# Kernel optimization log

Measured on AMD Instinct MI355X. Metric: run time of the kernel, lower is better.

The kernel has to match this reference:

```python
import jax, jax.numpy as jnp
import numpy as np

IN_CH = 64
OUT_CH = 64
SEQ_LEN = 2048
MODES = 64  # modes2 = min(modes1, seq_len//2) = 64
SCALE = 1.0 / (IN_CH * OUT_CH)


def setup_inputs() -> dict:
    key = jax.random.key(0)
    k1, k2, k3 = jax.random.split(key, 3)
    x = jax.random.normal(k1, (32, 8, IN_CH, SEQ_LEN), dtype=jnp.float32)
    # torch.rand(...) complex init scaled by 1/(in*out): real & imag in [0, scale)
    wr = SCALE * jax.random.uniform(k2, (IN_CH, OUT_CH, MODES), dtype=jnp.float32)
    wi = SCALE * jax.random.uniform(k3, (IN_CH, OUT_CH, MODES), dtype=jnp.float32)
    return {"x": x, "wr": wr, "wi": wi}


def reference(x, wr, wi):
    # x: [B, H, E, N] real; weights complex [in, out, modes]
    N = x.shape[-1]
    w = jax.lax.complex(wr, wi)
    x_ft = jnp.fft.rfft(x)                       # [B, H, E, N//2+1] complex64
    a = x_ft[..., :MODES]                        # keep only low modes
    out_low = jnp.einsum('bjix,iox->bjox', a, w)  # per-mode complex matmul
    # zero-fill remaining frequency bins (equivalent to out_ft zeros + slice set)
    pad = N // 2 + 1 - MODES
    out_ft = jnp.pad(out_low, ((0, 0), (0, 0), (0, 0), (0, pad)))
    return jnp.fft.irfft(out_ft, n=N)            # [B, H, out_ch, N] real
```

## Files before the change

### kernel.cpp

```cpp
#include <hip/hip_runtime.h>
#include <hip/hip_bf16.h>


typedef __bf16 bf16x8 __attribute__((ext_vector_type(8)));
typedef float  f32x4  __attribute__((ext_vector_type(4)));

#define SEQ 2048
#define NM2 128
#define KS  2

__device__ __forceinline__ unsigned int rnbf(float f) {
  unsigned int u = __builtin_bit_cast(unsigned int, f);
  return (u + 0x7fffu + ((u >> 16) & 1u)) >> 16;
}
__device__ __forceinline__ unsigned int pack2(float a, float b) {
  return rnbf(a) | (rnbf(b) << 16);
}
__device__ __forceinline__ float frombf(unsigned int lo16_in_place) {
  return __builtin_bit_cast(float, lo16_in_place);
}

typedef const __attribute__((address_space(1))) unsigned int gu32;
typedef __attribute__((address_space(3))) unsigned int lu32;

__global__ __launch_bounds__(256) void k_tables(unsigned short* __restrict__ t1sw,
                                                unsigned short* __restrict__ t2t) {
  int idx = blockIdx.x * 256 + threadIdx.x;
  int k = idx >> 11;
  int n = idx & 2047;
  float rev = (float)((k * n) & 2047) * (1.0f / 2048.0f);
  float s, co;
  asm("v_sin_f32 %0, %1" : "=v"(s)  : "v"(rev));
  asm("v_cos_f32 %0, %1" : "=v"(co) : "v"(rev));
  float ck = (k == 0 ? 1.0f : 2.0f) * (1.0f / 2048.0f);
  int kt = n >> 6, part = (n >> 3) & 7, e = n & 7;
  unsigned base = (unsigned)kt * 16384u + 2u * (unsigned)e;
  unsigned offc = base + (((unsigned)(k * 128 + part * 16)) ^ (((unsigned)k & 7u) << 4));
  int c2 = k + 64;
  unsigned offs = base + (((unsigned)(c2 * 128 + part * 16)) ^ (((unsigned)c2 & 7u) << 4));
  *(unsigned short*)((char*)t1sw + offc) = (unsigned short)rnbf(co);
  *(unsigned short*)((char*)t1sw + offs) = (unsigned short)rnbf(-s);
  t2t[n * NM2 + k]      = (unsigned short)rnbf(ck * co);
  t2t[n * NM2 + k + 64] = (unsigned short)rnbf(-ck * s);
}

__global__ __launch_bounds__(256) void k_gemm1(const float* __restrict__ x,
                                               const unsigned short* __restrict__ t1sw,
                                               unsigned short* __restrict__ P) {
  __shared__ int4 lds4[65536 / 16];
  char* lds = (char*)lds4;
  const int tid = threadIdx.x, wave = tid >> 6, lane = tid & 63;
  const int mtile = blockIdx.x >> 1, ks = blockIdx.x & (KS - 1);
  const int r0 = mtile * 64;
  const int kbase = ks * (SEQ / KS);
  const char* t1base = (const char*)t1sw + (size_t)(kbase >> 6) * 16384;

  const float* xsrc[4];
#pragma unroll
  for (int p = 0; p < 4; ++p) {
    const int row = p * 16 + wave * 4 + (lane >> 4);
    const int u = (lane & 15) ^ (row & 7);
    xsrc[p] = x + (size_t)(r0 + row) * SEQ + kbase + u * 4;
  }

  f32x4 acc[8] = {};

#pragma unroll
  for (int p = 0; p < 4; ++p)
    __builtin_amdgcn_global_load_lds((gu32*)(xsrc[p]),
                                     (lu32*)(lds + p * 4096 + wave * 1024), 16, 0, 0);
#pragma unroll
  for (int p = 0; p < 4; ++p)
    __builtin_amdgcn_global_load_lds((gu32*)(t1base + (p * 256 + tid) * 16),
                                     (lu32*)(lds + 32768 + (p * 256 + wave * 64) * 16), 16, 0, 0);
  asm volatile("s_waitcnt vmcnt(0)" ::: "memory");
  __builtin_amdgcn_s_barrier();

  const int a = wave * 16 + (lane & 15);
  const unsigned xra = (unsigned)(a & 7) << 4;
  const int kg = lane >> 4;

  for (int it = 0; it < 16; ++it) {
    const int cur = it & 1, nxt = cur ^ 1;
    const int xoff = cur * 16384;
    const int toff = 32768 + cur * 16384;
    if (it < 15) {
      const char* tg = t1base + (size_t)(it + 1) * 16384;
#pragma unroll
      for (int p = 0; p < 4; ++p)
        __builtin_amdgcn_global_load_lds((gu32*)(xsrc[p] + (it + 1) * 64),
                                         (lu32*)(lds + nxt * 16384 + p * 4096 + wave * 1024),
                                         16, 0, 0);
#pragma unroll
      for (int p = 0; p < 4; ++p)
        __builtin_amdgcn_global_load_lds((gu32*)(tg + (p * 256 + tid) * 16),
                                         (lu32*)(lds + 32768 + nxt * 16384 + (p * 256 + wave * 64) * 16),
                                         16, 0, 0);
    }
#pragma unroll
    for (int kss = 0; kss < 2; ++kss) {
      const unsigned byte0 = (unsigned)(a * 256 + kss * 128 + kg * 32);
      const f32x4 lo = *(const f32x4*)(lds + xoff + (byte0 ^ xra));
      const f32x4 hi = *(const f32x4*)(lds + xoff + ((byte0 + 16) ^ xra));
      unsigned c0, c1, c2, c3;
      asm("v_cvt_pk_bf16_f32 %0, %1, %2" : "=v"(c0) : "v"(lo[0]), "v"(lo[1]));
      asm("v_cvt_pk_bf16_f32 %0, %1, %2" : "=v"(c1) : "v"(lo[2]), "v"(lo[3]));
      asm("v_cvt_pk_bf16_f32 %0, %1, %2" : "=v"(c2) : "v"(hi[0]), "v"(hi[1]));
      asm("v_cvt_pk_bf16_f32 %0, %1, %2" : "=v"(c3) : "v"(hi[2]), "v"(hi[3]));
      uint4 pk; pk.x = c0; pk.y = c1; pk.z = c2; pk.w = c3;
      const bf16x8 av = __builtin_bit_cast(bf16x8, pk);
#pragma unroll
      for (int t = 0; t < 8; ++t) {
        const int col = t * 16 + (lane & 15);
        const bf16x8 bv = *(const bf16x8*)(lds + toff +
            ((col * 128 + kss * 64 + kg * 16) ^ ((unsigned)(col & 7) << 4)));
        acc[t] = __builtin_amdgcn_mfma_f32_16x16x32_bf16(bv, av, acc[t], 0, 0, 0);
      }
    }
    asm volatile("s_waitcnt vmcnt(0)" ::: "memory");
    __builtin_amdgcn_s_barrier();
  }
  unsigned short* Pout = P + (size_t)ks * (16384 * NM2);
  const int row = r0 + wave * 16 + (lane & 15);
#pragma unroll
  for (int t = 0; t < 8; ++t) {
    const int col0 = t * 16 + kg * 4;
    uint2 v; v.x = pack2(acc[t][0], acc[t][1]); v.y = pack2(acc[t][2], acc[t][3]);
    *(uint2*)(Pout + (size_t)row * NM2 + col0) = v;
  }
}

__global__ __launch_bounds__(256) void k_stage2(const unsigned short* __restrict__ P,
                                                const float* __restrict__ wr,
                                                const float* __restrict__ wi,
                                                unsigned short* __restrict__ Bx) {
  __shared__ float sA[4][64][64];
  const int b = blockIdx.x;
  const int bjc = b >> 2, oh = (b >> 1) & 1, kh = b & 1;
  const int k0 = kh * 32;
  const int tid = threadIdx.x;
#pragma unroll
  for (int p = 0; p < 16; ++p) {
    int fidx = tid + 256 * p;
    int row_lin = fidx >> 4, q = fidx & 15;
    int col = (q < 8) ? (k0 + q * 4) : (64 + k0 + (q - 8) * 4);
    const unsigned short* base = P + (size_t)(bjc * 256 + row_lin) * NM2 + col;
    f32x4 v = {};
#pragma unroll
    for (int s = 0; s < KS; ++s) {
      uint2 u = *(const uint2*)(base + (size_t)s * (16384 * NM2));
      v[0] += frombf(u.x << 16);
      v[1] += frombf(u.x & 0xffff0000u);
      v[2] += frombf(u.y << 16);
      v[3] += frombf(u.y & 0xffff0000u);
    }
    *(f32x4*)(&sA[row_lin >> 6][row_lin & 63][q * 4]) = v;
  }
  __syncthreads();
  const int o_l = tid >> 3, kg = tid & 7;
  const int o = oh * 32 + o_l;
  const int kb = k0 + kg * 4;
  f32x4 accr[4] = {};
  f32x4 acci[4] = {};
  for (int i = 0; i < 64; ++i) {
    f32x4 wrv = *(const f32x4*)(wr + (i * 64 + o) * 64 + kb);
    f32x4 wiv = *(const f32x4*)(wi + (i * 64 + o) * 64 + kb);
#pragma unroll
    for (int bj = 0; bj < 4; ++bj) {
      f32x4 ar = *(const f32x4*)(&sA[bj][i][kg * 4]);
      f32x4 ai = *(const f32x4*)(&sA[bj][i][32 + kg * 4]);
#pragma unroll
      for (int kk = 0; kk < 4; ++kk) {
        accr[bj][kk] += ar[kk] * wrv[kk] - ai[kk] * wiv[kk];
        acci[bj][kk] += ar[kk] * wiv[kk] + ai[kk] * wrv[kk];
      }
    }
  }
#pragma unroll
  for (int bj = 0; bj < 4; ++bj) {
    const int r = (bjc * 4 + bj) * 64 + o;
    uint2 vr; vr.x = pack2(accr[bj][0], accr[bj][1]); vr.y = pack2(accr[bj][2], accr[bj][3]);
    uint2 vi; vi.x = pack2(acci[bj][0], acci[bj][1]); vi.y = pack2(acci[bj][2], acci[bj][3]);
    *(uint2*)(Bx + (size_t)r * NM2 + kb)      = vr;
    *(uint2*)(Bx + (size_t)r * NM2 + 64 + kb) = vi;
  }
}

__global__ __launch_bounds__(256) void k_gemm2(const unsigned short* __restrict__ Bx,
                                               const unsigned short* __restrict__ t2t,
                                               float* __restrict__ out) {
  __shared__ int4 lds4[65536 / 16];
  char* lds = (char*)lds4;
  const int tid = threadIdx.x, wave = tid >> 6, lane = tid & 63;
  const int swz = (blockIdx.x & 7) * 256 + (blockIdx.x >> 3);
  const int mb = swz >> 4, nb = swz & 15;
  const int r0 = mb * 128, n0 = nb * 128;
#pragma unroll
  for (int p = 0; p < 8; ++p) {
    int seg = tid + 256 * p;
    int row = seg >> 4, part = seg & 15;
    unsigned sw = (unsigned)((row * 256 + part * 16) ^ ((row & 7) << 4));
    int4 va = *(const int4*)(Bx + (size_t)(r0 + row) * NM2 + part * 8);
    *(int4*)(lds + sw) = va;
    int4 vb = *(const int4*)(t2t + (size_t)(n0 + row) * NM2 + part * 8);
    *(int4*)(lds + 32768 + sw) = vb;
  }
  __syncthreads();
  f32x4 acc[2][8] = {};
#pragma unroll
  for (int ks = 0; ks < 4; ++ks) {
    const int ar0 = wave * 32 + (lane & 15);
    const int ar1 = ar0 + 16;
    const int koff = ks * 64 + (lane >> 4) * 16;
    bf16x8 a0 = *(const bf16x8*)(lds + ((ar0 * 256 + koff) ^ ((unsigned)(ar0 & 7) << 4)));
    bf16x8 a1 = *(const bf16x8*)(lds + ((ar1 * 256 + koff) ^ ((unsigned)(ar1 & 7) << 4)));
#pragma unroll
    for (int t = 0; t < 8; ++t) {
      const int col = t * 16 + (lane & 15);
      bf16x8 bv = *(const bf16x8*)(lds + 32768 + ((col * 256 + koff) ^ ((unsigned)(col & 7) << 4)));
      acc[0][t] = __builtin_amdgcn_mfma_f32_16x16x32_bf16(a0, bv, acc[0][t], 0, 0, 0);
      acc[1][t] = __builtin_amdgcn_mfma_f32_16x16x32_bf16(a1, bv, acc[1][t], 0, 0, 0);
    }
  }
#pragma unroll
  for (int m = 0; m < 2; ++m) {
#pragma unroll
    for (int j = 0; j < 4; ++j) {
      const int row = r0 + wave * 32 + m * 16 + (lane >> 4) * 4 + j;
#pragma unroll
      for (int t = 0; t < 8; ++t) {
        const int col = n0 + t * 16 + (lane & 15);
        out[(size_t)row * SEQ + col] = acc[m][t][j];
      }
    }
  }
}

extern "C" void kernel_launch(void* const* d_in, const int* in_sizes, int n_in,
                              void* d_out, int out_size, void* d_ws, size_t ws_size,
                              hipStream_t stream) {
  const float* x  = (const float*)d_in[0];
  const float* wr = (const float*)d_in[1];
  const float* wi = (const float*)d_in[2];
  float* out = (float*)d_out;
  char* ws = (char*)d_ws;
  unsigned short* t1sw = (unsigned short*)(ws);
  unsigned short* t2t  = (unsigned short*)(ws + 524288);
  unsigned short* P    = (unsigned short*)(ws + 1048576);
  unsigned short* Bx   = (unsigned short*)(ws + 1048576 + (size_t)KS * 16384 * NM2 * 2);

  k_tables<<<dim3(512),      dim3(256), 0, stream>>>(t1sw, t2t);
  k_gemm1 <<<dim3(256 * KS), dim3(256), 0, stream>>>(x, t1sw, P);
  k_stage2<<<dim3(256),      dim3(256), 0, stream>>>(P, wr, wi, Bx);
  k_gemm2 <<<dim3(2048),     dim3(256), 0, stream>>>(Bx, t2t, out);
}
```

Before: 89.48 us.

## Pre-swizzle gemm2 operands in global memory and load them directly to LDS

The Bx and t2 tables are now written in a tile-contiguous, pre-swizzled layout that matches the LDS image k_gemm2 needs, with real and imaginary halves in separate 16KB blocks. k_gemm2 then fills LDS with global_load_lds DMA instead of register round-trips. It waits only for the first half (vmcnt(8)) before starting MFMAs on it, overlapping the second half's load with compute. This couples the producer layouts tightly to gemm2's tiling and relies on the DMA lane-to-LDS mapping matching the swizzle.

```diff
diff --git a/kernel.cpp b/kernel.cpp
--- a/kernel.cpp
+++ b/kernel.cpp
@@ -24,7 +24,7 @@
 typedef __attribute__((address_space(3))) unsigned int lu32;
 
 __global__ __launch_bounds__(256) void k_tables(unsigned short* __restrict__ t1sw,
-                                                unsigned short* __restrict__ t2t) {
+                                                unsigned short* __restrict__ t2sw) {
   int idx = blockIdx.x * 256 + threadIdx.x;
   int k = idx >> 11;
   int n = idx & 2047;
@@ -33,15 +33,22 @@
   asm("v_sin_f32 %0, %1" : "=v"(s)  : "v"(rev));
   asm("v_cos_f32 %0, %1" : "=v"(co) : "v"(rev));
   float ck = (k == 0 ? 1.0f : 2.0f) * (1.0f / 2048.0f);
-  int kt = n >> 6, part = (n >> 3) & 7, e = n & 7;
-  unsigned base = (unsigned)kt * 16384u + 2u * (unsigned)e;
-  unsigned offc = base + (((unsigned)(k * 128 + part * 16)) ^ (((unsigned)k & 7u) << 4));
-  int c2 = k + 64;
-  unsigned offs = base + (((unsigned)(c2 * 128 + part * 16)) ^ (((unsigned)c2 & 7u) << 4));
-  *(unsigned short*)((char*)t1sw + offc) = (unsigned short)rnbf(co);
-  *(unsigned short*)((char*)t1sw + offs) = (unsigned short)rnbf(-s);
-  t2t[n * NM2 + k]      = (unsigned short)rnbf(ck * co);
-  t2t[n * NM2 + k + 64] = (unsigned short)rnbf(-ck * s);
+  {
+    int kt = n >> 6, part = (n >> 3) & 7, e = n & 7;
+    unsigned base = (unsigned)kt * 16384u + 2u * (unsigned)e;
+    unsigned offc = base + (((unsigned)(k * 128 + part * 16)) ^ (((unsigned)k & 7u) << 4));
+    int c2 = k + 64;
+    unsigned offs = base + (((unsigned)(c2 * 128 + part * 16)) ^ (((unsigned)c2 & 7u) << 4));
+    *(unsigned short*)((char*)t1sw + offc) = (unsigned short)rnbf(co);
+    *(unsigned short*)((char*)t1sw + offs) = (unsigned short)rnbf(-s);
+  }
+  {
+    int tile = n >> 7, rl = n & 127;
+    unsigned rowbase = (unsigned)tile * 32768u + (unsigned)rl * 128u;
+    unsigned kpart = ((((unsigned)(k >> 3)) * 16u) ^ (((unsigned)rl & 7u) << 4)) + 2u * ((unsigned)k & 7u);
+    *(unsigned short*)((char*)t2sw + rowbase + kpart)          = (unsigned short)rnbf(ck * co);
+    *(unsigned short*)((char*)t2sw + rowbase + 16384u + kpart) = (unsigned short)rnbf(-ck * s);
+  }
 }
 
 __global__ __launch_bounds__(256) void k_gemm1(const float* __restrict__ x,
@@ -133,7 +140,7 @@
 __global__ __launch_bounds__(256) void k_stage2(const unsigned short* __restrict__ P,
                                                 const float* __restrict__ wr,
                                                 const float* __restrict__ wi,
-                                                unsigned short* __restrict__ Bx) {
+                                                char* __restrict__ Bxsw) {
   __shared__ float sA[4][64][64];
   const int b = blockIdx.x;
   const int bjc = b >> 2, oh = (b >> 1) & 1, kh = b & 1;
@@ -179,15 +186,18 @@
 #pragma unroll
   for (int bj = 0; bj < 4; ++bj) {
     const int r = (bjc * 4 + bj) * 64 + o;
+    const int tile = r >> 7, rl = r & 127;
+    char* bb = Bxsw + (size_t)tile * 32768 + (size_t)rl * 128;
+    const unsigned kp = ((((unsigned)kb >> 3) * 16u) ^ (((unsigned)rl & 7u) << 4)) + 2u * ((unsigned)kb & 7u);
     uint2 vr; vr.x = pack2(accr[bj][0], accr[bj][1]); vr.y = pack2(accr[bj][2], accr[bj][3]);
     uint2 vi; vi.x = pack2(acci[bj][0], acci[bj][1]); vi.y = pack2(acci[bj][2], acci[bj][3]);
-    *(uint2*)(Bx + (size_t)r * NM2 + kb)      = vr;
-    *(uint2*)(Bx + (size_t)r * NM2 + 64 + kb) = vi;
-  }
-}
-
-__global__ __launch_bounds__(256) void k_gemm2(const unsigned short* __restrict__ Bx,
-                                               const unsigned short* __restrict__ t2t,
+    *(uint2*)(bb + kp)          = vr;
+    *(uint2*)(bb + 16384 + kp)  = vi;
+  }
+}
+
+__global__ __launch_bounds__(256) void k_gemm2(const char* __restrict__ Bxsw,
+                                               const char* __restrict__ t2sw,
                                                float* __restrict__ out) {
   __shared__ int4 lds4[65536 / 16];
   char* lds = (char*)lds4;
@@ -195,31 +205,53 @@
   const int swz = (blockIdx.x & 7) * 256 + (blockIdx.x >> 3);
   const int mb = swz >> 4, nb = swz & 15;
   const int r0 = mb * 128, n0 = nb * 128;
-#pragma unroll
-  for (int p = 0; p < 8; ++p) {
-    int seg = tid + 256 * p;
-    int row = seg >> 4, part = seg & 15;
-    unsigned sw = (unsigned)((row * 256 + part * 16) ^ ((row & 7) << 4));
-    int4 va = *(const int4*)(Bx + (size_t)(r0 + row) * NM2 + part * 8);
-    *(int4*)(lds + sw) = va;
-    int4 vb = *(const int4*)(t2t + (size_t)(n0 + row) * NM2 + part * 8);
-    *(int4*)(lds + 32768 + sw) = vb;
-  }
-  __syncthreads();
+  const char* bsrc = Bxsw + (size_t)mb * 32768;
+  const char* tsrc = t2sw + (size_t)nb * 32768;
+#pragma unroll
+  for (int i = 0; i < 4; ++i)
+    __builtin_amdgcn_global_load_lds((gu32*)(bsrc + i * 4096 + tid * 16),
+                                     (lu32*)(lds + i * 4096 + wave * 1024), 16, 0, 0);
+#pragma unroll
+  for (int i = 0; i < 4; ++i)
+    __builtin_amdgcn_global_load_lds((gu32*)(tsrc + i * 4096 + tid * 16),
+                                     (lu32*)(lds + 32768 + i * 4096 + wave * 1024), 16, 0, 0);
+#pragma unroll
+  for (int i = 0; i < 4; ++i)
+    __builtin_amdgcn_global_load_lds((gu32*)(bsrc + 16384 + i * 4096 + tid * 16),
+                                     (lu32*)(lds + 16384 + i * 4096 + wave * 1024), 16, 0, 0);
+#pragma unroll
+  for (int i = 0; i < 4; ++i)
+    __builtin_amdgcn_global_load_lds((gu32*)(tsrc + 16384 + i * 4096 + tid * 16),
+                                     (lu32*)(lds + 49152 + i * 4096 + wave * 1024), 16, 0, 0);
+  asm volatile("s_waitcnt vmcnt(8)" ::: "memory");
+  __builtin_amdgcn_s_barrier();
+
   f32x4 acc[2][8] = {};
-#pragma unroll
-  for (int ks = 0; ks < 4; ++ks) {
-    const int ar0 = wave * 32 + (lane & 15);
-    const int ar1 = ar0 + 16;
-    const int koff = ks * 64 + (lane >> 4) * 16;
-    bf16x8 a0 = *(const bf16x8*)(lds + ((ar0 * 256 + koff) ^ ((unsigned)(ar0 & 7) << 4)));
-    bf16x8 a1 = *(const bf16x8*)(lds + ((ar1 * 256 + koff) ^ ((unsigned)(ar1 & 7) << 4)));
-#pragma unroll
-    for (int t = 0; t < 8; ++t) {
-      const int col = t * 16 + (lane & 15);
-      bf16x8 bv = *(const bf16x8*)(lds + 32768 + ((col * 256 + koff) ^ ((unsigned)(col & 7) << 4)));
-      acc[0][t] = __builtin_amdgcn_mfma_f32_16x16x32_bf16(a0, bv, acc[0][t], 0, 0, 0);
-      acc[1][t] = __builtin_amdgcn_mfma_f32_16x16x32_bf16(a1, bv, acc[1][t], 0, 0, 0);
+  const int rowA0 = wave * 32 + (lane & 15);
+  const int rowA1 = rowA0 + 16;
+  const unsigned xa0 = (unsigned)(rowA0 & 7) << 4;
+  const unsigned xa1 = (unsigned)(rowA1 & 7) << 4;
+
+#pragma unroll
+  for (int half = 0; half < 2; ++half) {
+    if (half == 1) {
+      asm volatile("s_waitcnt vmcnt(0)" ::: "memory");
+      __builtin_amdgcn_s_barrier();
+    }
+    const int ab = half * 16384;
+    const int bb = 32768 + half * 16384;
+#pragma unroll
+    for (int kq = 0; kq < 2; ++kq) {
+      const unsigned offh = (unsigned)(kq * 64 + (lane >> 4) * 16);
+      const bf16x8 a0 = *(const bf16x8*)(lds + ab + rowA0 * 128 + (offh ^ xa0));
+      const bf16x8 a1 = *(const bf16x8*)(lds + ab + rowA1 * 128 + (offh ^ xa1));
+#pragma unroll
+      for (int t = 0; t < 8; ++t) {
+        const int rn = t * 16 + (lane & 15);
+        const bf16x8 bv = *(const bf16x8*)(lds + bb + rn * 128 + (offh ^ ((unsigned)(rn & 7) << 4)));
+        acc[0][t] = __builtin_amdgcn_mfma_f32_16x16x32_bf16(a0, bv, acc[0][t], 0, 0, 0);
+        acc[1][t] = __builtin_amdgcn_mfma_f32_16x16x32_bf16(a1, bv, acc[1][t], 0, 0, 0);
+      }
     }
   }
 #pragma unroll
@@ -245,12 +277,12 @@
   float* out = (float*)d_out;
   char* ws = (char*)d_ws;
   unsigned short* t1sw = (unsigned short*)(ws);
-  unsigned short* t2t  = (unsigned short*)(ws + 524288);
+  unsigned short* t2sw = (unsigned short*)(ws + 524288);
   unsigned short* P    = (unsigned short*)(ws + 1048576);
-  unsigned short* Bx   = (unsigned short*)(ws + 1048576 + (size_t)KS * 16384 * NM2 * 2);
-
-  k_tables<<<dim3(512),      dim3(256), 0, stream>>>(t1sw, t2t);
+  char*           Bxsw = (char*)(ws + 1048576 + (size_t)KS * 16384 * NM2 * 2);
+
+  k_tables<<<dim3(512),      dim3(256), 0, stream>>>(t1sw, t2sw);
   k_gemm1 <<<dim3(256 * KS), dim3(256), 0, stream>>>(x, t1sw, P);
-  k_stage2<<<dim3(256),      dim3(256), 0, stream>>>(P, wr, wi, Bx);
-  k_gemm2 <<<dim3(2048),     dim3(256), 0, stream>>>(Bx, t2t, out);
-}
+  k_stage2<<<dim3(256),      dim3(256), 0, stream>>>(P, wr, wi, Bxsw);
+  k_gemm2 <<<dim3(2048),     dim3(256), 0, stream>>>(Bxsw, (const char*)t2sw, out);
+}
```

After: 90.50 us. About the same (+1.1%).
